# Kernel optimization log

Hardware: AMD Instinct MI355X
Metric: run time of the kernel (lower is better)

Reference implementation:

```python
import jax, jax.numpy as jnp
import numpy as np

NEG_SLOPE = 0.2  # PyG GATv2 leaky_relu slope
LN_EPS = 1e-5


def _layernorm(x, gamma, beta):
    mu = x.mean(-1, keepdims=True)
    var = x.var(-1, keepdims=True)
    return (x - mu) * jax.lax.rsqrt(var + LN_EPS) * gamma + beta


def _gatv2_conv(x, src, dst, eattr, Wl, Wr, We, att, bias, concat):
    """PyG GATv2Conv (eval mode). x:(N,F), src/dst:(E,), eattr:(E,edge_dim), att:(H,C)."""
    N = x.shape[0]
    H, C = att.shape
    xl = (x @ Wl).reshape(N, H, C)   # source transform (messages)
    xr = (x @ Wr).reshape(N, H, C)   # target transform
    e = (eattr @ We).reshape(-1, H, C)
    m = xl[src] + xr[dst] + e                                   # (E,H,C)
    score = jnp.sum(jax.nn.leaky_relu(m, NEG_SLOPE) * att, -1)  # (E,H)
    # segment softmax over incoming edges per destination node
    smax = jax.ops.segment_max(score, dst, num_segments=N)
    ex = jnp.exp(score - smax[dst])
    denom = jax.ops.segment_sum(ex, dst, num_segments=N)
    alpha = ex / (denom[dst] + 1e-16)                           # (E,H)
    out = jax.ops.segment_sum(alpha[:, :, None] * xl[src], dst, num_segments=N)  # (N,H,C)
    out = out.reshape(N, H * C) if concat else out.mean(axis=1)
    return out + bias


def setup_inputs() -> dict:
    key = jax.random.key(0)
    ks = jax.random.split(key, 20)
    N, E = 10000, 320000
    D, HID, HEADS, ED = 256, 128, 4, 4
    HC = HID * HEADS  # 512

    def w(k, fi, fo):
        return jax.random.normal(k, (fi, fo), jnp.float32) / np.sqrt(fi)

    x = jax.random.normal(ks[0], (N, D), jnp.float32)
    edge_index = jax.random.randint(ks[1], (2, E), 0, N, jnp.int64)
    edge_attr = jax.random.normal(ks[2], (E, ED), jnp.float32)
    return {
        "x": x, "edge_index": edge_index, "edge_attr": edge_attr,
        # layer 1: heads=4, concat=True
        "Wl1": w(ks[3], D, HC), "Wr1": w(ks[4], D, HC), "We1": w(ks[5], ED, HC),
        "att1": jax.random.normal(ks[6], (HEADS, HID), jnp.float32) / np.sqrt(HID),
        "b1": jnp.zeros((HC,), jnp.float32),
        "g1": jnp.ones((HC,), jnp.float32), "be1": jnp.zeros((HC,), jnp.float32),
        # layer 2: heads=1, concat=False
        "Wl2": w(ks[7], HC, D), "Wr2": w(ks[8], HC, D), "We2": w(ks[9], ED, D),
        "att2": jax.random.normal(ks[10], (1, D), jnp.float32) / np.sqrt(D),
        "b2": jnp.zeros((D,), jnp.float32),
        "g2": jnp.ones((D,), jnp.float32), "be2": jnp.zeros((D,), jnp.float32),
    }


def reference(x, edge_index, edge_attr,
              Wl1, Wr1, We1, att1, b1, g1, be1,
              Wl2, Wr2, We2, att2, b2, g2, be2):
    N = x.shape[0]
    # PyG default add_self_loops=True with edge_attr fill_value='mean'
    loop = jnp.arange(N, dtype=edge_index.dtype)
    src = jnp.concatenate([edge_index[0], loop])
    dst = jnp.concatenate([edge_index[1], loop])
    ea = jnp.concatenate([edge_attr, jnp.broadcast_to(edge_attr.mean(0), (N, edge_attr.shape[1]))])

    h = _gatv2_conv(x, src, dst, ea, Wl1, Wr1, We1, att1, b1, concat=True)
    h = _layernorm(h, g1, be1)
    h = jax.nn.elu(h)  # dropout is identity in eval mode

    h = _gatv2_conv(h, src, dst, ea, Wl2, Wr2, We2, att2, b2, concat=False)
    h = _layernorm(h, g2, be2)
    return h + x  # residual (in_channels == out_channels)
```

## Files before the change

### kernel.cpp

```cpp
#include <hip/hip_runtime.h>
#include <hip/hip_bf16.h>

#define HC1 512
#define HC2 256
#define D_IN 256
#define CAP  128

typedef __hip_bfloat16  bf16;
typedef __hip_bfloat162 bf162;
typedef __attribute__((ext_vector_type(8))) short short8;
typedef __attribute__((ext_vector_type(4))) float f32x4;
typedef __attribute__((ext_vector_type(2))) float f32x2;

__device__ __forceinline__ void unpack8p(short8 q, f32x2* xa) {
  union { short8 s; unsigned u[4]; } uu; uu.s = q;
#pragma unroll
  for (int j = 0; j < 4; j++) {
    union { unsigned u; float f; } lo, hi;
    lo.u = uu.u[j] << 16;
    hi.u = uu.u[j] & 0xffff0000u;
    xa[j].x = lo.f; xa[j].y = hi.f;
  }
}
__device__ __forceinline__ void load8p(const float* p, f32x2* d) {
  float4 a = *(const float4*)p, b = *(const float4*)(p + 4);
  d[0].x = a.x; d[0].y = a.y; d[1].x = a.z; d[1].y = a.w;
  d[2].x = b.x; d[2].y = b.y; d[3].x = b.z; d[3].y = b.w;
}

template <int CTRL>
__device__ __forceinline__ float dppadd(float x) {
  union { float f; int i; } u, v;
  u.f = x;
  v.i = __builtin_amdgcn_update_dpp(0, u.i, CTRL, 0xF, 0xF, true);
  return x + v.f;
}
__device__ __forceinline__ float red16(float p) {
  p = dppadd<0xB1>(p);
  p = dppadd<0x4E>(p);
  p = dppadd<0x124>(p);
  p = dppadd<0x128>(p);
  return p;
}

__device__ __forceinline__ void glds16(const bf16* g, bf16* l) {
#if __has_builtin(__builtin_amdgcn_global_load_lds)
  __builtin_amdgcn_global_load_lds(
      (const __attribute__((address_space(1))) void*)g,
      (__attribute__((address_space(3))) void*)l, 16, 0, 0);
#else
  int lane = threadIdx.x & 63;
  ((int4*)l)[lane] = *(const int4*)g;
#endif
}

__global__ __launch_bounds__(256)
void gemm_mfma_kernel(const bf16* __restrict__ A, const bf16* __restrict__ BT,
                      bf16* __restrict__ C, int M, int K, int N) {
  __shared__ bf16 lds[8192];
  const int t = threadIdx.x;
  const int w  = t >> 6, l = t & 63;
  const int wr = w >> 1, wc = w & 1;
  const int lo = l & 15, hi = l >> 4;
  const int m0 = blockIdx.y * 128;
  const int n0 = blockIdx.x * 128;

  f32x4 acc[4][4] = {};

  const int c0 = w * 2, c1 = w * 2 + 1;
  const int kc0 = c0 >> 1, r0 = (c0 & 1) * 64 + l;
  const int kc1 = c1 >> 1, r1 = (c1 & 1) * 64 + l;
  int mr0 = m0 + r0; if (mr0 >= M) mr0 = M - 1;
  int mr1 = m0 + r1; if (mr1 >= M) mr1 = M - 1;
  const bf16* ga0 = A + (size_t)mr0 * K + kc0 * 8;
  const bf16* ga1 = A + (size_t)mr1 * K + kc1 * 8;
  const bf16* gb0 = BT + (size_t)(n0 + r0) * K + kc0 * 8;
  const bf16* gb1 = BT + (size_t)(n0 + r1) * K + kc1 * 8;
  bf16* la0 = &lds[c0 * 512];
  bf16* la1 = &lds[c1 * 512];
  bf16* lb0 = &lds[4096 + c0 * 512];
  bf16* lb1 = &lds[4096 + c1 * 512];

  for (int k0 = 0; k0 < K; k0 += 32) {
    if (k0) __syncthreads();
    glds16(ga0 + k0, la0);
    glds16(ga1 + k0, la1);
    glds16(gb0 + k0, lb0);
    glds16(gb1 + k0, lb1);
    __syncthreads();

    short8 af[4], bfr[4];
#pragma unroll
    for (int f = 0; f < 4; f++) {
      af[f]  = *(const short8*)&lds[hi * 1024 + (wr * 64 + f * 16 + lo) * 8];
      bfr[f] = *(const short8*)&lds[4096 + hi * 1024 + (wc * 64 + f * 16 + lo) * 8];
    }
#pragma unroll
    for (int fm = 0; fm < 4; fm++)
#pragma unroll
      for (int fn = 0; fn < 4; fn++)
        acc[fm][fn] = __builtin_amdgcn_mfma_f32_16x16x32_bf16(af[fm], bfr[fn],
                                                              acc[fm][fn], 0, 0, 0);
  }

#pragma unroll
  for (int fm = 0; fm < 4; fm++) {
#pragma unroll
    for (int r = 0; r < 4; r++) {
      int row = m0 + wr * 64 + fm * 16 + hi * 4 + r;
      if (row < M) {
#pragma unroll
        for (int fn = 0; fn < 4; fn++) {
          int col = n0 + wc * 64 + fn * 16 + lo;
          C[(size_t)row * N + col] = __float2bfloat16(acc[fm][fn][r]);
        }
      }
    }
  }
}

__global__ void convx_kernel(const float* __restrict__ x, bf16* __restrict__ xb, int n4) {
  int i = blockIdx.x * blockDim.x + threadIdx.x;
  if (i >= n4) return;
  float4 v = ((const float4*)x)[i];
  union { bf16 h[4]; uint2 u; } cv;
  cv.h[0] = __float2bfloat16(v.x); cv.h[1] = __float2bfloat16(v.y);
  cv.h[2] = __float2bfloat16(v.z); cv.h[3] = __float2bfloat16(v.w);
  ((uint2*)xb)[i] = cv.u;
}

__global__ __launch_bounds__(256)
void transw_kernel(const float* __restrict__ Wl1, const float* __restrict__ Wr1,
                   const float* __restrict__ Wl2, const float* __restrict__ Wr2,
                   bf16* __restrict__ W1T, bf16* __restrict__ W2T) {
  __shared__ float tile[32][33];
  const int z = blockIdx.z;
  const float* in; bf16* out; int K, Nn;
  if (z == 0)      { in = Wl1; out = W1T;             K = 256; Nn = 512; }
  else if (z == 1) { in = Wr1; out = W1T + 512 * 256; K = 256; Nn = 512; }
  else if (z == 2) { in = Wl2; out = W2T;             K = 512; Nn = 256; }
  else             { in = Wr2; out = W2T + 256 * 512; K = 512; Nn = 256; }
  const int nt = blockIdx.x * 32, kt = blockIdx.y * 32;
  if (nt >= Nn || kt >= K) return;
  const int tx = threadIdx.x & 31, ty = threadIdx.x >> 5;
#pragma unroll
  for (int j = 0; j < 4; j++)
    tile[ty + j * 8][tx] = in[(size_t)(kt + ty + j * 8) * Nn + nt + tx];
  __syncthreads();
#pragma unroll
  for (int j = 0; j < 4; j++)
    out[(size_t)(nt + ty + j * 8) * K + kt + tx] = __float2bfloat16(tile[tx][ty + j * 8]);
}

__global__ __launch_bounds__(256)
void fill_kernel(const int* __restrict__ ei, const float* __restrict__ eattr,
                 int* __restrict__ cnt, int* __restrict__ srcs,
                 float4* __restrict__ eaC, float* __restrict__ sums, int E) {
  __shared__ float4 bred[4];
  int tid = blockIdx.x * blockDim.x + threadIdx.x;
  int stride = gridDim.x * blockDim.x;
  float l0 = 0.f, l1 = 0.f, l2 = 0.f, l3 = 0.f;
  for (int e = tid; e < E; e += stride) {
    int src = ei[e], dst = ei[E + e];
    float4 ea = ((const float4*)eattr)[e];
    int pos = atomicAdd(&cnt[dst], 1);
    if (pos < CAP) {
      int slot = dst * CAP + pos;
      srcs[slot] = src;
      eaC[slot] = ea;
    }
    l0 += ea.x; l1 += ea.y; l2 += ea.z; l3 += ea.w;
  }
#pragma unroll
  for (int o = 1; o < 64; o <<= 1) {
    l0 += __shfl_xor(l0, o); l1 += __shfl_xor(l1, o);
    l2 += __shfl_xor(l2, o); l3 += __shfl_xor(l3, o);
  }
  int wave = threadIdx.x >> 6, lane = threadIdx.x & 63;
  if (lane == 0) bred[wave] = make_float4(l0, l1, l2, l3);
  __syncthreads();
  if (threadIdx.x == 0) {
    float4 a = bred[0], b = bred[1], c = bred[2], d = bred[3];
    atomicAdd(&sums[0], a.x + b.x + c.x + d.x);
    atomicAdd(&sums[1], a.y + b.y + c.y + d.y);
    atomicAdd(&sums[2], a.z + b.z + c.z + d.z);
    atomicAdd(&sums[3], a.w + b.w + c.w + d.w);
  }
}

__global__ void meanw_kernel(const float* __restrict__ sums, float* __restrict__ mean4, float invE) {
  int t = threadIdx.x;
  if (t < 4) mean4[t] = sums[t] * invE;
}

__global__ __launch_bounds__(256, 4)
void fused1_kernel(const int* __restrict__ srcs, const float4* __restrict__ eaC,
                   const int* __restrict__ cnt, const float* __restrict__ mean4,
                   const bf16* __restrict__ xlr,
                   const float* __restrict__ We, const float* __restrict__ att,
                   const float* __restrict__ bias, const float* __restrict__ g,
                   const float* __restrict__ be, bf16* __restrict__ h1) {
  const int v = blockIdx.x;
  const int tid = threadIdx.x;
  const int wave = tid >> 6, lane = tid & 63;
  const int ch = lane * 8;

  f32x2 w0p[4], w1p[4], w2p[4], w3p[4], awp[4], xrp[4];
  load8p(We + 0 * HC1 + ch, w0p);
  load8p(We + 1 * HC1 + ch, w1p);
  load8p(We + 2 * HC1 + ch, w2p);
  load8p(We + 3 * HC1 + ch, w3p);
  load8p(att + ch, awp);
  unpack8p(*(const short8*)(xlr + (size_t)v * 1024 + 512 + ch), xrp);

  int len = cnt[v]; if (len > CAP) len = CAP;
  const int beg = v * CAP, end = beg + len;
  const int chunk = (len + 3) >> 2;
  int ib = beg + wave * chunk;
  int ie = ib + chunk;
  if (ib > end) ib = end;
  if (ie > end) ie = end;

  float den = 0.f;
  f32x2 accp[4] = {};

  auto edge = [&](short8 q, float4 e) {
    f32x2 xa[4]; unpack8p(q, xa);
    f32x2 p2 = {0.f, 0.f};
#pragma unroll
    for (int j = 0; j < 4; j++) {
      f32x2 m = xa[j] + xrp[j];
      m += e.x * w0p[j];
      m += e.y * w1p[j];
      m += e.z * w2p[j];
      m += e.w * w3p[j];
      f32x2 lm = __builtin_elementwise_max(m, m * 0.2f);
      p2 += lm * awp[j];
    }
    float p = p2.x + p2.y;
    p = red16(p);
    float ex = __expf(p);
    den += ex;
#pragma unroll
    for (int j = 0; j < 4; j++) accp[j] += xa[j] * ex;
  };

  int i = ib;
  for (; i + 4 <= ie; i += 4) {
    int s0 = srcs[i], s1 = srcs[i + 1], s2 = srcs[i + 2], s3 = srcs[i + 3];
    float4 e0 = eaC[i], e1 = eaC[i + 1], e2 = eaC[i + 2], e3 = eaC[i + 3];
    short8 q0 = *(const short8*)(xlr + (size_t)s0 * 1024 + ch);
    short8 q1 = *(const short8*)(xlr + (size_t)s1 * 1024 + ch);
    short8 q2 = *(const short8*)(xlr + (size_t)s2 * 1024 + ch);
    short8 q3 = *(const short8*)(xlr + (size_t)s3 * 1024 + ch);
    edge(q0, e0); edge(q1, e1); edge(q2, e2); edge(q3, e3);
  }
  for (; i < ie; ++i) {
    int s0 = srcs[i];
    float4 e0 = eaC[i];
    short8 q0 = *(const short8*)(xlr + (size_t)s0 * 1024 + ch);
    edge(q0, e0);
  }
  if (wave == 0) {
    float4 e0 = *(const float4*)mean4;
    short8 q0 = *(const short8*)(xlr + (size_t)v * 1024 + ch);
    edge(q0, e0);
  }

  __shared__ float accs[4][HC1];
  __shared__ float dens[4][4];
  __shared__ float2 red[4];
  *(float4*)&accs[wave][ch]     = *(float4*)&accp[0];
  *(float4*)&accs[wave][ch + 4] = *(float4*)&accp[2];
  if ((lane & 15) == 0) dens[wave][lane >> 4] = den;
  __syncthreads();

  const int c = tid * 2;
  const int head = c >> 7;
  const float dtot = dens[0][head] + dens[1][head] + dens[2][head] + dens[3][head];
  const float rden = 1.f / (dtot + 1e-16f);
  float2 a0 = *(float2*)&accs[0][c];
  float2 a1 = *(float2*)&accs[1][c];
  float2 a2 = *(float2*)&accs[2][c];
  float2 a3 = *(float2*)&accs[3][c];
  float2 bv = *(const float2*)(bias + c);
  float val0 = (a0.x + a1.x + a2.x + a3.x) * rden + bv.x;
  float val1 = (a0.y + a1.y + a2.y + a3.y) * rden + bv.y;

  float s1 = val0 + val1, s2 = val0 * val0 + val1 * val1;
  s1 = red16(s1); s2 = red16(s2);
  s1 += __shfl_xor(s1, 16); s2 += __shfl_xor(s2, 16);
  s1 += __shfl_xor(s1, 32); s2 += __shfl_xor(s2, 32);
  if (lane == 0) red[wave] = make_float2(s1, s2);
  __syncthreads();
  float ts1 = red[0].x + red[1].x + red[2].x + red[3].x;
  float ts2 = red[0].y + red[1].y + red[2].y + red[3].y;
  float mu  = ts1 * (1.f / HC1);
  float var = ts2 * (1.f / HC1) - mu * mu;
  float rs  = rsqrtf(var + 1e-5f);

  float2 gv = *(const float2*)(g + c);
  float2 ev = *(const float2*)(be + c);
  float ya = (val0 - mu) * rs * gv.x + ev.x;
  float yb = (val1 - mu) * rs * gv.y + ev.y;
  ya = (ya > 0.f) ? ya : expm1f(ya);
  yb = (yb > 0.f) ? yb : expm1f(yb);
  bf162 hv;
  hv.x = __float2bfloat16(ya); hv.y = __float2bfloat16(yb);
  *(bf162*)(h1 + (size_t)v * HC1 + c) = hv;
}

__global__ __launch_bounds__(256, 3)
void fused2_kernel(const int* __restrict__ srcs, const float4* __restrict__ eaC,
                   const int* __restrict__ cnt, const float* __restrict__ mean4,
                   const bf16* __restrict__ xlr,
                   const float* __restrict__ We, const float* __restrict__ att,
                   const float* __restrict__ bias, const float* __restrict__ g,
                   const float* __restrict__ be, const float* __restrict__ xin,
                   float* __restrict__ out) {
  const int v = blockIdx.x;
  const int tid = threadIdx.x;
  const int wave = tid >> 6, lane = tid & 63;
  const int half = lane >> 5;
  const int hl = lane & 31;
  const int c0 = hl * 8;

  f32x2 w0p[4], w1p[4], w2p[4], w3p[4], atp[4], xrp[4];
  load8p(We + 0 * HC2 + c0, w0p);
  load8p(We + 1 * HC2 + c0, w1p);
  load8p(We + 2 * HC2 + c0, w2p);
  load8p(We + 3 * HC2 + c0, w3p);
  load8p(att + c0, atp);
  unpack8p(*(const short8*)(xlr + (size_t)v * 512 + 256 + c0), xrp);

  int len = cnt[v]; if (len > CAP) len = CAP;
  const int beg = v * CAP, end = beg + len;
  const int chunk = (len + 3) >> 2;
  int ib = beg + wave * chunk;
  int ie = ib + chunk;
  if (ib > end) ib = end;
  if (ie > end) ie = end;

  float den = 0.f;
  f32x2 accp[4] = {};

  auto pair = [&](short8 q, float4 e, bool bvalid) {
    f32x2 xa[4]; unpack8p(q, xa);
    f32x2 p2 = {0.f, 0.f};
#pragma unroll
    for (int j = 0; j < 4; j++) {
      f32x2 m = xa[j] + xrp[j];
      m += e.x * w0p[j];
      m += e.y * w1p[j];
      m += e.z * w2p[j];
      m += e.w * w3p[j];
      f32x2 lm = __builtin_elementwise_max(m, m * 0.2f);
      p2 += lm * atp[j];
    }
    float p = p2.x + p2.y;
    p = red16(p);
    p += __shfl_xor(p, 16);
    float ex = __expf(p);
    if (half && !bvalid) ex = 0.f;
    den += ex;
#pragma unroll
    for (int j = 0; j < 4; j++) accp[j] += xa[j] * ex;
  };

  int i = ib;
  for (; i + 4 <= ie; i += 4) {
    int sA = srcs[i + half],   sB = srcs[i + 2 + half];
    float4 eA = eaC[i + half], eB = eaC[i + 2 + half];
    short8 qA = *(const short8*)(xlr + (size_t)sA * 512 + c0);
    short8 qB = *(const short8*)(xlr + (size_t)sB * 512 + c0);
    pair(qA, eA, true); pair(qB, eB, true);
  }
  for (; i < ie; i += 2) {
    bool hasB = (i + 1 < ie);
    int idx = i + half; if (idx > ie - 1) idx = i;
    int s = srcs[idx];
    float4 e = eaC[idx];
    short8 q = *(const short8*)(xlr + (size_t)s * 512 + c0);
    pair(q, e, hasB);
  }
  if (wave == 0) {
    float4 e = *(const float4*)mean4;
    short8 q = *(const short8*)(xlr + (size_t)v * 512 + c0);
    pair(q, e, false);
  }

#pragma unroll
  for (int j = 0; j < 4; j++) {
    accp[j].x += __shfl_xor(accp[j].x, 32);
    accp[j].y += __shfl_xor(accp[j].y, 32);
  }
  den += __shfl_xor(den, 32);

  __shared__ float accs[4][HC2];
  __shared__ float dens[4];
  __shared__ float2 red[4];
  if (half == 0) {
    *(float4*)&accs[wave][c0]     = *(float4*)&accp[0];
    *(float4*)&accs[wave][c0 + 4] = *(float4*)&accp[2];
  }
  if (lane == 0) dens[wave] = den;
  __syncthreads();

  const int c = tid;
  const float dtot = dens[0] + dens[1] + dens[2] + dens[3];
  const float rden = 1.f / (dtot + 1e-16f);
  float val = (accs[0][c] + accs[1][c] + accs[2][c] + accs[3][c]) * rden + bias[c];

  float s1 = val, s2 = val * val;
  s1 = red16(s1); s2 = red16(s2);
  s1 += __shfl_xor(s1, 16); s2 += __shfl_xor(s2, 16);
  s1 += __shfl_xor(s1, 32); s2 += __shfl_xor(s2, 32);
  if (lane == 0) red[wave] = make_float2(s1, s2);
  __syncthreads();
  float ts1 = red[0].x + red[1].x + red[2].x + red[3].x;
  float ts2 = red[0].y + red[1].y + red[2].y + red[3].y;
  float mu  = ts1 * (1.f / HC2);
  float var = ts2 * (1.f / HC2) - mu * mu;
  float rs  = rsqrtf(var + 1e-5f);
  float y = (val - mu) * rs * g[c] + be[c];
  out[(size_t)v * HC2 + c] = y + xin[(size_t)v * HC2 + c];
}

extern "C" void kernel_launch(void* const* d_in, const int* in_sizes, int n_in,
                              void* d_out, int out_size, void* d_ws, size_t ws_size,
                              hipStream_t stream) {
  const float* x     = (const float*)d_in[0];
  const int*   ei    = (const int*)d_in[1];
  const float* eattr = (const float*)d_in[2];
  const float* Wl1   = (const float*)d_in[3];
  const float* Wr1   = (const float*)d_in[4];
  const float* We1   = (const float*)d_in[5];
  const float* att1  = (const float*)d_in[6];
  const float* b1    = (const float*)d_in[7];
  const float* g1    = (const float*)d_in[8];
  const float* be1   = (const float*)d_in[9];
  const float* Wl2   = (const float*)d_in[10];
  const float* Wr2   = (const float*)d_in[11];
  const float* We2   = (const float*)d_in[12];
  const float* att2  = (const float*)d_in[13];
  const float* b2    = (const float*)d_in[14];
  const float* g2    = (const float*)d_in[15];
  const float* be2   = (const float*)d_in[16];

  const int N    = in_sizes[0] / D_IN;
  const int E    = in_sizes[2] / 4;

  char* w = (char*)d_ws;
  auto alloc = [&](size_t bytes) -> void* {
    void* p = (void*)w;
    w += (bytes + 255) & ~(size_t)255;
    return p;
  };
  bf16*   xb    = (bf16*)alloc((size_t)N * D_IN * 2);
  bf16*   W1T   = (bf16*)alloc((size_t)1024 * 256 * 2);
  bf16*   W2T   = (bf16*)alloc((size_t)512 * 512 * 2);
  bf16*   xlr1  = (bf16*)alloc((size_t)N * 1024 * 2);
  bf16*   h1    = (bf16*)alloc((size_t)N * HC1 * 2);
  bf16*   xlr2  = (bf16*)alloc((size_t)N * 512 * 2);
  int*    srcs  = (int*)alloc((size_t)N * CAP * 4);
  float4* eaC   = (float4*)alloc((size_t)N * CAP * 16);
  float*  mean4 = (float*)alloc(64);
  char*   zb    = w;
  int*    cnt   = (int*)alloc((size_t)N * 4);
  float*  sums  = (float*)alloc(64);
  size_t  zbytes = (size_t)(w - zb);

  hipMemsetAsync(zb, 0, zbytes, stream);

  int n4 = N * D_IN / 4;
  convx_kernel<<<(n4 + 255) / 256, 256, 0, stream>>>(x, xb, n4);
  transw_kernel<<<dim3(16, 16, 4), 256, 0, stream>>>(Wl1, Wr1, Wl2, Wr2, W1T, W2T);

  fill_kernel<<<1024, 256, 0, stream>>>(ei, eattr, cnt, srcs, eaC, sums, E);
  meanw_kernel<<<1, 64, 0, stream>>>(sums, mean4, 1.f / (float)E);

  dim3 gg1(1024 / 128, (N + 127) / 128);
  gemm_mfma_kernel<<<gg1, 256, 0, stream>>>(xb, W1T, xlr1, N, 256, 1024);

  fused1_kernel<<<N, 256, 0, stream>>>(srcs, eaC, cnt, mean4, xlr1, We1, att1,
                                       b1, g1, be1, h1);

  dim3 gg2(512 / 128, (N + 127) / 128);
  gemm_mfma_kernel<<<gg2, 256, 0, stream>>>(h1, W2T, xlr2, N, 512, 512);

  fused2_kernel<<<N, 256, 0, stream>>>(srcs, eaC, cnt, mean4, xlr2, We2, att2,
                                       b2, g2, be2, x, (float*)d_out);
}
```

Measured before the change: 243.2 us.

## Double-buffer edge gathers via global-to-LDS async loads in fused1 kernel

Replaces the per-iteration register gathers of source-node features in fused1_kernel with a double-buffered pipeline. Each wave issues direct global-to-LDS loads (glds16) for the next four edges while it computes on the current four from shared memory, using explicit vmcnt waits and scheduling barriers. This aims to hide gather latency behind compute, at the cost of 32KB of extra LDS per block, which may reduce occupancy. It also relies on the glds16 helper and manual waitcnt accounting being correct.

```diff
diff --git a/kernel.cpp b/kernel.cpp
--- a/kernel.cpp
+++ b/kernel.cpp
@@ -205,6 +205,9 @@
   const int wave = tid >> 6, lane = tid & 63;
   const int ch = lane * 8;
 
+  __shared__ bf16 stage[4][2][4][512];
+  bf16* stw = &stage[wave][0][0][0];
+
   f32x2 w0p[4], w1p[4], w2p[4], w3p[4], awp[4], xrp[4];
   load8p(We + 0 * HC1 + ch, w0p);
   load8p(We + 1 * HC1 + ch, w1p);
@@ -246,14 +249,44 @@
   };
 
   int i = ib;
-  for (; i + 4 <= ie; i += 4) {
+  if (i + 4 <= ie) {
     int s0 = srcs[i], s1 = srcs[i + 1], s2 = srcs[i + 2], s3 = srcs[i + 3];
-    float4 e0 = eaC[i], e1 = eaC[i + 1], e2 = eaC[i + 2], e3 = eaC[i + 3];
-    short8 q0 = *(const short8*)(xlr + (size_t)s0 * 1024 + ch);
-    short8 q1 = *(const short8*)(xlr + (size_t)s1 * 1024 + ch);
-    short8 q2 = *(const short8*)(xlr + (size_t)s2 * 1024 + ch);
-    short8 q3 = *(const short8*)(xlr + (size_t)s3 * 1024 + ch);
-    edge(q0, e0); edge(q1, e1); edge(q2, e2); edge(q3, e3);
+    float4 ec0 = eaC[i], ec1 = eaC[i + 1], ec2 = eaC[i + 2], ec3 = eaC[i + 3];
+    __builtin_amdgcn_sched_barrier(0);
+    glds16(xlr + (size_t)s0 * 1024 + ch, stw);
+    glds16(xlr + (size_t)s1 * 1024 + ch, stw + 512);
+    glds16(xlr + (size_t)s2 * 1024 + ch, stw + 1024);
+    glds16(xlr + (size_t)s3 * 1024 + ch, stw + 1536);
+    i += 4;
+    int cur = 0;
+    for (;;) {
+      bf16* stc = cur ? (stw + 2048) : stw;
+      const bool more = (i + 4 <= ie);
+      float4 en0, en1, en2, en3;
+      if (more) {
+        int t0 = srcs[i], t1 = srcs[i + 1], t2 = srcs[i + 2], t3 = srcs[i + 3];
+        en0 = eaC[i]; en1 = eaC[i + 1]; en2 = eaC[i + 2]; en3 = eaC[i + 3];
+        __builtin_amdgcn_sched_barrier(0);
+        bf16* stn = cur ? stw : (stw + 2048);
+        glds16(xlr + (size_t)t0 * 1024 + ch, stn);
+        glds16(xlr + (size_t)t1 * 1024 + ch, stn + 512);
+        glds16(xlr + (size_t)t2 * 1024 + ch, stn + 1024);
+        glds16(xlr + (size_t)t3 * 1024 + ch, stn + 1536);
+        asm volatile("s_waitcnt vmcnt(4)" ::: "memory");
+      } else {
+        asm volatile("s_waitcnt vmcnt(0)" ::: "memory");
+      }
+      __builtin_amdgcn_sched_barrier(0);
+      short8 q0 = *(const short8*)(stc + lane * 8);
+      short8 q1 = *(const short8*)(stc + 512 + lane * 8);
+      short8 q2 = *(const short8*)(stc + 1024 + lane * 8);
+      short8 q3 = *(const short8*)(stc + 1536 + lane * 8);
+      edge(q0, ec0); edge(q1, ec1); edge(q2, ec2); edge(q3, ec3);
+      if (!more) break;
+      ec0 = en0; ec1 = en1; ec2 = en2; ec3 = en3;
+      cur ^= 1;
+      i += 4;
+    }
   }
   for (; i < ie; ++i) {
     int s0 = srcs[i];
```

New measurement: 257.1 us. 5.7% more time.
